# Optimization experiments

Hardware: AMD Instinct MI355X
Metric: run time of the kernel (lower is better)

## Reference

```python
import jax, jax.numpy as jnp
import numpy as np

NUM_ITERATIONS = 3
NUM_ROUTES = 6912  # 32*6*6*6


def _squash(t):
    # t: [..., O]; squash along last dim
    sq = jnp.sum(t * t, axis=-1, keepdims=True)
    return sq * t / ((1.0 + sq) * jnp.sqrt(sq))


def setup_inputs() -> dict:
    key = jax.random.key(0)
    k1, k2 = jax.random.split(key)
    B, R, I, C, O = 64, NUM_ROUTES, 8, 10, 16
    x = jax.random.normal(k1, (B, R, I), dtype=jnp.float32)
    route_weights = jax.random.normal(k2, (C, R, I, O), dtype=jnp.float32)
    return {"x": x, "route_weights": route_weights}


def reference(x, route_weights):
    # x: [B, R, I]; route_weights: [C, R, I, O]
    # priors = x[None,:,:,None,:] @ W[:,None,:,:,:] -> [C, B, R, 1, O]
    priors = jnp.einsum('bri,crio->cbro', x, route_weights)[:, :, :, None, :]
    logits = jnp.zeros_like(priors)  # [C, B, R, 1, O]
    outputs = None
    for i in range(NUM_ITERATIONS):
        # softmax over routes (dim=2), matching custom softmax(input, dim=2)
        probs = jax.nn.softmax(logits, axis=2)
        outputs = _squash(jnp.sum(probs * priors, axis=2, keepdims=True))  # [C,B,1,1,O]
        if i != NUM_ROUTES - 1:  # always true in original (num_routes >> iters)
            delta = jnp.sum(priors * outputs, axis=-1, keepdims=True)  # [C,B,R,1,1]
            logits = logits + delta
    return outputs
```

## Files before the change

### kernel.cpp

```cpp
#include <hip/hip_runtime.h>
#include <math.h>

#define BB 64
#define RR 6912
#define II 8
#define CC 10
#define OO 16
#define RPB2 96
#define NCH2 72
#define NG2 12
#define NBLK 720
#define MRG_PAD 20
#define WTILE_I4 (RPB2*16)
#define MRGF (4*64*MRG_PAD + 4*64)
#define PWW (CC*NCH2*BB*OO)
#define PZW (CC*NCH2*BB)
#define L_ARR(c)      ((c) * 32)
#define L_ARREP(c,r)  ((10 + (c)*8 + (r)) * 32)
#define L_CD(c)       ((90 + (c)) * 32)
#define L_RD(c,r)     ((100 + (c)*8 + (r)) * 32)
#define FLAGI (180*32)

typedef _Float16 h2 __attribute__((ext_vector_type(2)));
typedef _Float16 half8 __attribute__((ext_vector_type(8)));
typedef float f32x16 __attribute__((ext_vector_type(16)));
union HV { int4 v; h2 h[4]; half8 h8; };

__device__ __forceinline__ void xchf(float* p, float v) {
    float old = __hip_atomic_exchange(p, v, __ATOMIC_RELAXED, __HIP_MEMORY_SCOPE_AGENT);
    asm volatile("" :: "v"(old));
}
__device__ __forceinline__ void xchf2(float* p, float a, float b) {
    union { unsigned long long u; float f[2]; } v;
    v.f[0] = a; v.f[1] = b;
    unsigned long long old = __hip_atomic_exchange((unsigned long long*)p, v.u,
                              __ATOMIC_RELAXED, __HIP_MEMORY_SCOPE_AGENT);
    asm volatile("" :: "v"(old));
}
__device__ __forceinline__ int addi(int* p) {
    return __hip_atomic_fetch_add(p, 1, __ATOMIC_RELAXED, __HIP_MEMORY_SCOPE_AGENT);
}
__device__ __forceinline__ void xchi(int* p, int v) {
    int old = __hip_atomic_exchange(p, v, __ATOMIC_RELAXED, __HIP_MEMORY_SCOPE_AGENT);
    asm volatile("" :: "v"(old));
}
template <int SLP, int GUARD>
__device__ __forceinline__ void pollge(const int* p, int tgt) {
    int v = __hip_atomic_load(p, __ATOMIC_RELAXED, __HIP_MEMORY_SCOPE_AGENT);
    int g = 0;
    while (v < tgt && ++g < GUARD) {
        __builtin_amdgcn_s_sleep(SLP);
        v = __hip_atomic_load(p, __ATOMIC_RELAXED, __HIP_MEMORY_SCOPE_AGENT);
    }
}

__global__ __launch_bounds__(256) void prep_kernel(
    const float* __restrict__ x, int4* __restrict__ xth4,
    int* __restrict__ flags)
{
    __shared__ __align__(16) float4 lds4[64 * 34];
    const int t = threadIdx.x;
    const int bid = blockIdx.x;

    {
        const unsigned idx = (unsigned)bid * 256u + (unsigned)t;
        if (idx < (unsigned)FLAGI) flags[idx] = 0;
    }

    const int rblk = bid >> 2;
    const int bblk = bid & 3;
    const int r0 = rblk * 64, b0 = bblk * 16;
    {
        const int rl = t & 63;
        const int bl0 = t >> 6;
#pragma unroll
        for (int kb = 0; kb < 4; ++kb) {
            const int bl = kb * 4 + bl0;
            const float4* src = (const float4*)(x + ((size_t)(b0 + bl) * RR + (r0 + rl)) * II);
            lds4[rl * 34 + bl * 2 + 0] = src[0];
            lds4[rl * 34 + bl * 2 + 1] = src[1];
        }
    }
    __syncthreads();
    {
        const int bl = t & 15;
        const int rw0 = t >> 4;
#pragma unroll
        for (int kr = 0; kr < 4; ++kr) {
            const int rw = kr * 16 + rw0;
            float4 a = lds4[rw * 34 + bl * 2 + 0];
            float4 bq = lds4[rw * 34 + bl * 2 + 1];
            HV u;
            u.h[0] = h2{(_Float16)a.x,  (_Float16)a.y};
            u.h[1] = h2{(_Float16)a.z,  (_Float16)a.w};
            u.h[2] = h2{(_Float16)bq.x, (_Float16)bq.y};
            u.h[3] = h2{(_Float16)bq.z, (_Float16)bq.w};
            xth4[(size_t)(r0 + rw) * BB + (b0 + bl)] = u.v;
        }
    }
}

template <int MODE>
__device__ __forceinline__ void it_phase(
    const int4* __restrict__ xth4, const int4* wlds, float* mrg,
    const float* __restrict__ ov,
    float* __restrict__ pw, float* __restrict__ pz,
    int* flags, int c, int chunk, int xcd, int t, int ph)
{
    const int wv = t >> 6;
    const int l = t & 63;
    const int b = l & 31;
    const int hi = l >> 5;
    const int aquad = (l >> 4) & 1;
    const bool aact = (aquad == hi);

    if (MODE != 0) {
        if (t == 0) pollge<8, (1 << 14)>(flags + L_RD(c, xcd), ph - 1);
        __syncthreads();
    }

    float accA[8], accB[8];
#pragma unroll
    for (int j = 0; j < 8; ++j) { accA[j] = 0.f; accB[j] = 0.f; }
    float ZA = 0.f, ZB = 0.f;

    float ovA[8], ovB[8];
    if (MODE != 0) {
        const float* pa = ov + ((size_t)c * BB + b) * OO + 4 * hi;
        const float* pb = ov + ((size_t)c * BB + 32 + b) * OO + 4 * hi;
        float4 a0 = *(const float4*)(pa);
        float4 a1 = *(const float4*)(pa + 8);
        float4 b0 = *(const float4*)(pb);
        float4 b1 = *(const float4*)(pb + 8);
        ovA[0]=a0.x; ovA[1]=a0.y; ovA[2]=a0.z; ovA[3]=a0.w;
        ovA[4]=a1.x; ovA[5]=a1.y; ovA[6]=a1.z; ovA[7]=a1.w;
        ovB[0]=b0.x; ovB[1]=b0.y; ovB[2]=b0.z; ovB[3]=b0.w;
        ovB[4]=b1.x; ovB[5]=b1.y; ovB[6]=b1.z; ovB[7]=b1.w;
    }

    const int rbase = chunk * RPB2 + wv * 24;

    f32x16 cA, cB, zf;
#pragma unroll
    for (int q = 0; q < 16; ++q) { cA[q] = 0.f; cB[q] = 0.f; zf[q] = 0.f; }

    HV xc0, xc1, xn0, xn1;
    xc0.v = xth4[(size_t)(rbase + hi) * BB + b];
    xc1.v = xth4[(size_t)(rbase + hi) * BB + 32 + b];
    xn0 = xc0; xn1 = xc1;

#pragma unroll 1
    for (int g = 0; g < NG2; ++g) {
        if (g + 1 < NG2) {
            const int rn = rbase + (g + 1) * 2 + hi;
            xn0.v = xth4[(size_t)rn * BB + b];
            xn1.v = xth4[(size_t)rn * BB + 32 + b];
        }
        const int rl0 = wv * 24 + g * 2;
        HV wq;
        wq.v = wlds[(rl0 + aquad) * 16 + (l & 15)];
        if (!aact) wq.v = make_int4(0, 0, 0, 0);

        if (MODE == 0) {
            cA = __builtin_amdgcn_mfma_f32_32x32x16_f16(wq.h8, xc0.h8, cA, 0, 0, 0);
            cB = __builtin_amdgcn_mfma_f32_32x32x16_f16(wq.h8, xc1.h8, cB, 0, 0, 0);
        } else {
            f32x16 p0 = __builtin_amdgcn_mfma_f32_32x32x16_f16(wq.h8, xc0.h8, zf, 0, 0, 0);
            f32x16 p1 = __builtin_amdgcn_mfma_f32_32x32x16_f16(wq.h8, xc1.h8, zf, 0, 0, 0);
            float dA0 = 0.f, dA1 = 0.f, dB0 = 0.f, dB1 = 0.f;
#pragma unroll
            for (int j = 0; j < 8; ++j) {
                dA0 = fmaf(p0[j],     ovA[j], dA0);
                dA1 = fmaf(p0[j + 8], ovA[j], dA1);
                dB0 = fmaf(p1[j],     ovB[j], dB0);
                dB1 = fmaf(p1[j + 8], ovB[j], dB1);
            }
            dA0 += __shfl_xor(dA0, 32);
            dA1 += __shfl_xor(dA1, 32);
            dB0 += __shfl_xor(dB0, 32);
            dB1 += __shfl_xor(dB1, 32);
            const float eA0 = __expf(dA0), eA1 = __expf(dA1);
            const float eB0 = __expf(dB0), eB1 = __expf(dB1);
            ZA += eA0 + eA1; ZB += eB0 + eB1;
#pragma unroll
            for (int j = 0; j < 8; ++j) {
                accA[j] = fmaf(eA0, p0[j], fmaf(eA1, p0[j + 8], accA[j]));
                accB[j] = fmaf(eB0, p1[j], fmaf(eB1, p1[j + 8], accB[j]));
            }
        }
        xc0 = xn0; xc1 = xn1;
    }

    if (MODE == 0) {
#pragma unroll
        for (int j = 0; j < 8; ++j) {
            accA[j] = cA[j] + cA[j + 8];
            accB[j] = cB[j] + cB[j + 8];
        }
    }

    {
        float* m0 = mrg + (wv * 64 + b) * MRG_PAD + 4 * hi;
        *(float4*)(m0)     = make_float4(accA[0], accA[1], accA[2], accA[3]);
        *(float4*)(m0 + 8) = make_float4(accA[4], accA[5], accA[6], accA[7]);
        float* m1 = mrg + (wv * 64 + 32 + b) * MRG_PAD + 4 * hi;
        *(float4*)(m1)     = make_float4(accB[0], accB[1], accB[2], accB[3]);
        *(float4*)(m1 + 8) = make_float4(accB[4], accB[5], accB[6], accB[7]);
        if (MODE != 0 && hi == 0) {
            float* zr = mrg + 4 * 64 * MRG_PAD;
            zr[wv * 64 + b] = ZA;
            zr[wv * 64 + 32 + b] = ZB;
        }
    }
    __syncthreads();

    {
        const int b2 = t >> 2, q = t & 3;
        float4 sum = make_float4(0.f, 0.f, 0.f, 0.f);
#pragma unroll
        for (int w2 = 0; w2 < 4; ++w2) {
            const float4 v = *(const float4*)(mrg + (w2 * 64 + b2) * MRG_PAD + q * 4);
            sum.x += v.x; sum.y += v.y; sum.z += v.z; sum.w += v.w;
        }
        float* dst = pw + (((size_t)(c * BB + b2) * NCH2 + chunk) * OO) + q * 4;
        xchf2(dst + 0, sum.x, sum.y);
        xchf2(dst + 2, sum.z, sum.w);
        if (MODE != 0 && q == 0) {
            const float* zr = mrg + 4 * 64 * MRG_PAD;
            float z = 0.f;
#pragma unroll
            for (int w2 = 0; w2 < 4; ++w2) z += zr[w2 * 64 + b2];
            xchf(pz + (size_t)(c * BB + b2) * NCH2 + chunk, z);
        }
    }

    __syncthreads();
    if (t == 0) {
        const int old = addi(flags + L_ARR(c));
        if (old == NCH2 * ph - 1) {
#pragma unroll
            for (int r = 0; r < 8; ++r) xchi(flags + L_ARREP(c, r), ph);
        }
    }
}

template <int MODE>
__device__ __forceinline__ void combine_phase(
    const float* __restrict__ pw, const float* __restrict__ pzw,
    const float* __restrict__ addv, float* __restrict__ dst, bool coh,
    int* flags, int bid, int t, float* cl, int ph)
{
    const int c2 = bid >> 6, b2 = bid & 63;
    const int o = t & 15, g = t >> 4;

    if (t == 0) pollge<8, (1 << 14)>(flags + L_ARREP(c2, bid & 7), ph);
    __syncthreads();

    const float* base = pw + (size_t)(c2 * BB + b2) * NCH2 * OO;
    const float* zb   = pzw + (size_t)(c2 * BB + b2) * NCH2;
    float s = 0.f, zl = 0.f;
#pragma unroll
    for (int k = 0; k < 5; ++k) {
        const int rid = g + k * 16;
        if (rid < NCH2) {
            s += base[rid * OO + o];
            if (MODE != 0 && o == 0) zl += zb[rid];
        }
    }
    cl[t] = s;
    if (MODE != 0 && o == 0) cl[256 + g] = zl;
    __syncthreads();

    if (g == 0) {
#pragma unroll
        for (int k = 1; k < 16; ++k) s += cl[k * 16 + o];
        if (MODE != 0) {
            float Zt = 0.f;
#pragma unroll
            for (int k = 0; k < 16; ++k) Zt += cl[256 + k];
            s /= Zt;
        } else {
            s *= (1.0f / RR);
        }
        float sq = s * s;
#pragma unroll
        for (int w = 1; w < 16; w <<= 1) sq += __shfl_xor(sq, w);
        float val = s * sqrtf(sq) / (1.f + sq);
        if (MODE == 1) val += addv[(size_t)bid * OO + o];
        if (coh) xchf(dst + (size_t)bid * OO + o, val);
        else     dst[(size_t)bid * OO + o] = val;
    }
    __syncthreads();

    if (MODE != 2 && t == 0) {
        const int old = addi(flags + L_CD(c2));
        if (old == 64 * ph - 1) {
#pragma unroll
            for (int r = 0; r < 8; ++r) xchi(flags + L_RD(c2, r), ph);
        }
    }
}

__global__ __launch_bounds__(256, 3) void fused_kernel(
    const int4* __restrict__ xth4, const float* __restrict__ w,
    float* pw0, float* pw1, float* pw2, float* pz1, float* pz2,
    float* v0, float* outsum, float* out, int* flags)
{
    __shared__ __align__(16) int4 wlds[WTILE_I4];
    __shared__ __align__(16) float mrg[MRGF];
    __shared__ float cl[272];

    const int bid = blockIdx.x;
    const int t = threadIdx.x;
    const int xcd = bid & 7;
    const int u = xcd * 90 + (bid >> 3);
    const int chunk = u / 10;
    const int c = u - chunk * 10;

    {
        const float4* wsrc = (const float4*)(w + ((size_t)c * RR + (size_t)chunk * RPB2) * 128);
        _Float16* wl = (_Float16*)wlds;
        const int i  = (t >> 2) & 7;
        const int o0 = (t & 3) * 4;
#pragma unroll 6
        for (int p = 0; p < 12; ++p) {
            const float4 v = wsrc[p * 256 + t];
            const int rp = (p * 256 + t) >> 5;
            wl[(rp * 16 + o0 + 0) * 8 + i] = (_Float16)v.x;
            wl[(rp * 16 + o0 + 1) * 8 + i] = (_Float16)v.y;
            wl[(rp * 16 + o0 + 2) * 8 + i] = (_Float16)v.z;
            wl[(rp * 16 + o0 + 3) * 8 + i] = (_Float16)v.w;
        }
    }
    __syncthreads();

    it_phase<0>(xth4, wlds, mrg, nullptr, pw0, nullptr, flags, c, chunk, xcd, t, 1);
    if (bid < CC * BB) combine_phase<0>(pw0, nullptr, nullptr, v0, true, flags, bid, t, cl, 1);
    it_phase<1>(xth4, wlds, mrg, v0, pw1, pz1, flags, c, chunk, xcd, t, 2);
    if (bid < CC * BB) combine_phase<1>(pw1, pz1, v0, outsum, true, flags, bid, t, cl, 2);
    it_phase<2>(xth4, wlds, mrg, outsum, pw2, pz2, flags, c, chunk, xcd, t, 3);
    if (bid < CC * BB) combine_phase<2>(pw2, pz2, nullptr, out, false, flags, bid, t, cl, 3);
}

extern "C" void kernel_launch(void* const* d_in, const int* in_sizes, int n_in,
                              void* d_out, int out_size, void* d_ws, size_t ws_size,
                              hipStream_t stream)
{
    const float* x = (const float*)d_in[0];
    const float* w = (const float*)d_in[1];
    float* out = (float*)d_out;

    float* ws = (float*)d_ws;
    float* xth    = ws;
    float* pw0    = xth + (size_t)RR * BB * 4;
    float* pw1    = pw0 + PWW;
    float* pw2    = pw1 + PWW;
    float* pz1    = pw2 + PWW;
    float* pz2    = pz1 + PZW;
    float* v0     = pz2 + PZW;
    float* outsum = v0 + CC * BB * OO;
    int*   flags  = (int*)(outsum + CC * BB * OO);

    int4* xth4 = (int4*)xth;

    prep_kernel<<<dim3(432), dim3(256), 0, stream>>>(x, xth4, flags);
    fused_kernel<<<dim3(NBLK), dim3(256), 0, stream>>>(
        xth4, w, pw0, pw1, pw2, pz1, pz2, v0, outsum, out, flags);
}
```

Baseline: 133.7 us.

## Halve route chunk per block, double grid, and shrink LDS merge buffer

Halves the number of routes each block handles, so the grid doubles to 1440 blocks and the launch bound rises to 6 blocks per CU. The cross-wave merge buffer is cut in half by reducing in two passes (waves 0-1, then 2-3) with an extra barrier, which lowers LDS use enough to fit the higher occupancy. The aim is more resident blocks and more parallelism for this persistent, flag-synchronised kernel. In exchange there are twice as many partial sums for the combine step to reduce and twice as many blocks signalling the arrival counters, and the extra barriers add latency. Register pressure under the tighter launch bound may also cause spills.

```diff
diff --git a/kernel.cpp b/kernel.cpp
--- a/kernel.cpp
+++ b/kernel.cpp
@@ -6,13 +6,12 @@
 #define II 8
 #define CC 10
 #define OO 16
-#define RPB2 96
-#define NCH2 72
-#define NG2 12
-#define NBLK 720
+#define RPB2 48
+#define NCH2 144
+#define NG2 6
+#define NBLK 1440
 #define MRG_PAD 20
 #define WTILE_I4 (RPB2*16)
-#define MRGF (4*64*MRG_PAD + 4*64)
 #define PWW (CC*NCH2*BB*OO)
 #define PZW (CC*NCH2*BB)
 #define L_ARR(c)      ((c) * 32)
@@ -102,7 +101,7 @@
 
 template <int MODE>
 __device__ __forceinline__ void it_phase(
-    const int4* __restrict__ xth4, const int4* wlds, float* mrg,
+    const int4* __restrict__ xth4, const int4* wlds, float* mrg, float* zl,
     const float* __restrict__ ov,
     float* __restrict__ pw, float* __restrict__ pz,
     int* flags, int c, int chunk, int xcd, int t, int ph)
@@ -138,7 +137,7 @@
         ovB[4]=b1.x; ovB[5]=b1.y; ovB[6]=b1.z; ovB[7]=b1.w;
     }
 
-    const int rbase = chunk * RPB2 + wv * 24;
+    const int rbase = chunk * RPB2 + wv * (RPB2 / 4);
 
     f32x16 cA, cB, zf;
 #pragma unroll
@@ -156,7 +155,7 @@
             xn0.v = xth4[(size_t)rn * BB + b];
             xn1.v = xth4[(size_t)rn * BB + 32 + b];
         }
-        const int rl0 = wv * 24 + g * 2;
+        const int rl0 = wv * (RPB2 / 4) + g * 2;
         HV wq;
         wq.v = wlds[(rl0 + aquad) * 16 + (l & 15)];
         if (!aact) wq.v = make_int4(0, 0, 0, 0);
@@ -199,26 +198,42 @@
         }
     }
 
-    {
+    if (MODE != 0 && hi == 0) {
+        zl[wv * 64 + b] = ZA;
+        zl[wv * 64 + 32 + b] = ZB;
+    }
+    if (wv < 2) {
         float* m0 = mrg + (wv * 64 + b) * MRG_PAD + 4 * hi;
         *(float4*)(m0)     = make_float4(accA[0], accA[1], accA[2], accA[3]);
         *(float4*)(m0 + 8) = make_float4(accA[4], accA[5], accA[6], accA[7]);
         float* m1 = mrg + (wv * 64 + 32 + b) * MRG_PAD + 4 * hi;
         *(float4*)(m1)     = make_float4(accB[0], accB[1], accB[2], accB[3]);
         *(float4*)(m1 + 8) = make_float4(accB[4], accB[5], accB[6], accB[7]);
-        if (MODE != 0 && hi == 0) {
-            float* zr = mrg + 4 * 64 * MRG_PAD;
-            zr[wv * 64 + b] = ZA;
-            zr[wv * 64 + 32 + b] = ZB;
-        }
-    }
-    __syncthreads();
-
-    {
-        const int b2 = t >> 2, q = t & 3;
-        float4 sum = make_float4(0.f, 0.f, 0.f, 0.f);
-#pragma unroll
-        for (int w2 = 0; w2 < 4; ++w2) {
+    }
+    __syncthreads();
+
+    const int b2 = t >> 2, q = t & 3;
+    float4 sum = make_float4(0.f, 0.f, 0.f, 0.f);
+#pragma unroll
+    for (int w2 = 0; w2 < 2; ++w2) {
+        const float4 v = *(const float4*)(mrg + (w2 * 64 + b2) * MRG_PAD + q * 4);
+        sum.x += v.x; sum.y += v.y; sum.z += v.z; sum.w += v.w;
+    }
+    __syncthreads();
+
+    if (wv >= 2) {
+        float* m0 = mrg + ((wv - 2) * 64 + b) * MRG_PAD + 4 * hi;
+        *(float4*)(m0)     = make_float4(accA[0], accA[1], accA[2], accA[3]);
+        *(float4*)(m0 + 8) = make_float4(accA[4], accA[5], accA[6], accA[7]);
+        float* m1 = mrg + ((wv - 2) * 64 + 32 + b) * MRG_PAD + 4 * hi;
+        *(float4*)(m1)     = make_float4(accB[0], accB[1], accB[2], accB[3]);
+        *(float4*)(m1 + 8) = make_float4(accB[4], accB[5], accB[6], accB[7]);
+    }
+    __syncthreads();
+
+    {
+#pragma unroll
+        for (int w2 = 0; w2 < 2; ++w2) {
             const float4 v = *(const float4*)(mrg + (w2 * 64 + b2) * MRG_PAD + q * 4);
             sum.x += v.x; sum.y += v.y; sum.z += v.z; sum.w += v.w;
         }
@@ -226,10 +241,9 @@
         xchf2(dst + 0, sum.x, sum.y);
         xchf2(dst + 2, sum.z, sum.w);
         if (MODE != 0 && q == 0) {
-            const float* zr = mrg + 4 * 64 * MRG_PAD;
             float z = 0.f;
 #pragma unroll
-            for (int w2 = 0; w2 < 4; ++w2) z += zr[w2 * 64 + b2];
+            for (int w2 = 0; w2 < 4; ++w2) z += zl[w2 * 64 + b2];
             xchf(pz + (size_t)(c * BB + b2) * NCH2 + chunk, z);
         }
     }
@@ -260,12 +274,10 @@
     const float* zb   = pzw + (size_t)(c2 * BB + b2) * NCH2;
     float s = 0.f, zl = 0.f;
 #pragma unroll
-    for (int k = 0; k < 5; ++k) {
+    for (int k = 0; k < NCH2 / 16; ++k) {
         const int rid = g + k * 16;
-        if (rid < NCH2) {
-            s += base[rid * OO + o];
-            if (MODE != 0 && o == 0) zl += zb[rid];
-        }
+        s += base[rid * OO + o];
+        if (MODE != 0 && o == 0) zl += zb[rid];
     }
     cl[t] = s;
     if (MODE != 0 && o == 0) cl[256 + g] = zl;
@@ -301,19 +313,20 @@
     }
 }
 
-__global__ __launch_bounds__(256, 3) void fused_kernel(
+__global__ __launch_bounds__(256, 6) void fused_kernel(
     const int4* __restrict__ xth4, const float* __restrict__ w,
     float* pw0, float* pw1, float* pw2, float* pz1, float* pz2,
     float* v0, float* outsum, float* out, int* flags)
 {
     __shared__ __align__(16) int4 wlds[WTILE_I4];
-    __shared__ __align__(16) float mrg[MRGF];
+    __shared__ __align__(16) float mrg[2 * 64 * MRG_PAD];
+    __shared__ float zl[256];
     __shared__ float cl[272];
 
     const int bid = blockIdx.x;
     const int t = threadIdx.x;
     const int xcd = bid & 7;
-    const int u = xcd * 90 + (bid >> 3);
+    const int u = xcd * 180 + (bid >> 3);
     const int chunk = u / 10;
     const int c = u - chunk * 10;
 
@@ -322,8 +335,8 @@
         _Float16* wl = (_Float16*)wlds;
         const int i  = (t >> 2) & 7;
         const int o0 = (t & 3) * 4;
-#pragma unroll 6
-        for (int p = 0; p < 12; ++p) {
+#pragma unroll
+        for (int p = 0; p < 6; ++p) {
             const float4 v = wsrc[p * 256 + t];
             const int rp = (p * 256 + t) >> 5;
             wl[(rp * 16 + o0 + 0) * 8 + i] = (_Float16)v.x;
@@ -334,11 +347,11 @@
     }
     __syncthreads();
 
-    it_phase<0>(xth4, wlds, mrg, nullptr, pw0, nullptr, flags, c, chunk, xcd, t, 1);
+    it_phase<0>(xth4, wlds, mrg, zl, nullptr, pw0, nullptr, flags, c, chunk, xcd, t, 1);
     if (bid < CC * BB) combine_phase<0>(pw0, nullptr, nullptr, v0, true, flags, bid, t, cl, 1);
-    it_phase<1>(xth4, wlds, mrg, v0, pw1, pz1, flags, c, chunk, xcd, t, 2);
+    it_phase<1>(xth4, wlds, mrg, zl, v0, pw1, pz1, flags, c, chunk, xcd, t, 2);
     if (bid < CC * BB) combine_phase<1>(pw1, pz1, v0, outsum, true, flags, bid, t, cl, 2);
-    it_phase<2>(xth4, wlds, mrg, outsum, pw2, pz2, flags, c, chunk, xcd, t, 3);
+    it_phase<2>(xth4, wlds, mrg, zl, outsum, pw2, pz2, flags, c, chunk, xcd, t, 3);
     if (bid < CC * BB) combine_phase<2>(pw2, pz2, nullptr, out, false, flags, bid, t, cl, 3);
 }
 
```

Measured after the change: 195.1 us. 45.9% more time.
